# Kernel optimization log

Measured on AMD Instinct MI355X. Metric: run time of the kernel, lower is better.

The kernel has to match this reference:

```python
import jax, jax.numpy as jnp
import numpy as np

N_USERS = 200000
N_ITEMS = 100000
NNZ = 3000000
DIM = 128


def setup_inputs() -> dict:
    key = jax.random.key(0)
    k1, k2, k3, k4, k5 = jax.random.split(key, 5)
    user_emb = jax.random.normal(k1, (N_USERS, DIM), dtype=jnp.float32)
    item_emb = jax.random.normal(k2, (N_ITEMS, DIM), dtype=jnp.float32)
    mat_val = jax.random.uniform(k3, (NNZ,), dtype=jnp.float32)
    mat_row = jax.random.randint(k4, (NNZ,), 0, N_USERS, dtype=jnp.int32)
    mat_col = jax.random.randint(k5, (NNZ,), 0, N_ITEMS, dtype=jnp.int32)
    return {"user_emb": user_emb, "item_emb": item_emb, "mat_val": mat_val,
            "mat_row": mat_row, "mat_col": mat_col}


def reference(user_emb, item_emb, mat_val, mat_row, mat_col):
    # Bipartite SpMM, COO form (matches torch.sparse.mm in Aggregator.forward):
    # user_agg_cf = A @ item_emb,  A[u,i] = mat_val over edges (mat_row, mat_col)
    # item_agg_cf = A^T @ user_emb
    # messages: [nnz, DIM]
    u_msgs = mat_val[:, None] * item_emb[mat_col]
    user_agg_cf = jax.ops.segment_sum(u_msgs, mat_row, num_segments=N_USERS)
    i_msgs = mat_val[:, None] * user_emb[mat_row]
    item_agg_cf = jax.ops.segment_sum(i_msgs, mat_col, num_segments=N_ITEMS)
    return (user_agg_cf, item_agg_cf)
```

## Files before the change

kernel.cpp:

```cpp
#include <hip/hip_runtime.h>

#define N_USERS 200000
#define N_ITEMS 100000
#define NNZ     3000000
#define DIM     128
#define N_TOT   (N_USERS + N_ITEMS)

#define USEG_SH 8
#define ISEG_SH 7
#define NUB     ((N_USERS + (1 << USEG_SH) - 1) >> USEG_SH)
#define NIB     ((N_ITEMS + (1 << ISEG_SH) - 1) >> ISEG_SH)
#define NBKT    (NUB + NIB)
#define CAP     6144

#define NBR_BITS 18
#define NBR_MASK ((1 << NBR_BITS) - 1)

#define HDR_INTS_RAW ((N_TOT + 2) + (NBKT + 1) + NBKT)
#define HDR_INTS     ((HDR_INTS_RAW + 1) & ~1)
static const size_t WS_NEEDED = (size_t)HDR_INTS * 4 + (size_t)2 * NNZ * 8;


__global__ __launch_bounds__(256) void zero_buckets(int* __restrict__ bucketA) {
    int i = blockIdx.x * blockDim.x + threadIdx.x;
    if (i < NBKT + 1) bucketA[i] = 0;
}

#define HEPT 16
__global__ __launch_bounds__(256) void bucket_hist(const int* __restrict__ row,
                                                   const int* __restrict__ col,
                                                   int* __restrict__ bucketA) {
    __shared__ int h[NBKT];
    int t = threadIdx.x;
    for (int i = t; i < NBKT; i += 256) h[i] = 0;
    __syncthreads();
    int base = blockIdx.x * (256 * HEPT);
#pragma unroll
    for (int k = 0; k < HEPT; ++k) {
        int e = base + k * 256 + t;
        if (e < NNZ) {
            atomicAdd(&h[row[e] >> USEG_SH], 1);
            atomicAdd(&h[NUB + (col[e] >> ISEG_SH)], 1);
        }
    }
    __syncthreads();
    for (int i = t; i < NBKT; i += 256) {
        int c = h[i];
        if (c) atomicAdd(&bucketA[i], c);
    }
}

__global__ __launch_bounds__(256) void scan_buckets(int* __restrict__ bucketA,
                                                    int* __restrict__ gcur) {
    __shared__ int s[256];
    int t = threadIdx.x;
    int loc[8];
    int sum = 0;
#pragma unroll
    for (int k = 0; k < 8; ++k) {
        int i = t * 8 + k;
        int v = (i < NBKT) ? bucketA[i] : 0;
        loc[k] = v;
        sum += v;
    }
    s[t] = sum;
    __syncthreads();
    for (int o = 1; o < 256; o <<= 1) {
        int x = (t >= o) ? s[t - o] : 0;
        __syncthreads();
        s[t] += x;
        __syncthreads();
    }
    int ex = s[t] - sum;
#pragma unroll
    for (int k = 0; k < 8; ++k) {
        int i = t * 8 + k;
        if (i < NBKT) {
            bucketA[i] = ex;
            gcur[i] = ex;
            ex += loc[k];
        }
    }
    if (t == 255) bucketA[NBKT] = ex;
}

#define P1EPT 16
__global__ __launch_bounds__(256) void fill_pass1(const float* __restrict__ val,
                                                  const int* __restrict__ row,
                                                  const int* __restrict__ col,
                                                  int* __restrict__ gcur,
                                                  int2* __restrict__ stage) {
    __shared__ int h[NBKT];
    int t = threadIdx.x;
    for (int i = t; i < NBKT; i += 256) h[i] = 0;
    __syncthreads();
    int base = blockIdx.x * (256 * P1EPT);
    int r[P1EPT], c[P1EPT], vb[P1EPT];
#pragma unroll
    for (int k = 0; k < P1EPT; ++k) {
        int e = base + k * 256 + t;
        if (e < NNZ) {
            r[k] = row[e];
            c[k] = col[e];
            vb[k] = __float_as_int(val[e]);
            atomicAdd(&h[r[k] >> USEG_SH], 1);
            atomicAdd(&h[NUB + (c[k] >> ISEG_SH)], 1);
        } else {
            r[k] = -1;
        }
    }
    __syncthreads();
    for (int i = t; i < NBKT; i += 256) {
        int cc = h[i];
        h[i] = cc ? atomicAdd(&gcur[i], cc) : 0;
    }
    __syncthreads();
#pragma unroll
    for (int k = 0; k < P1EPT; ++k) {
        if (r[k] >= 0) {
            int b0 = r[k] >> USEG_SH;
            int p = atomicAdd(&h[b0], 1);
            stage[p] = make_int2(((r[k] & ((1 << USEG_SH) - 1)) << NBR_BITS) | c[k], vb[k]);
            int b1 = NUB + (c[k] >> ISEG_SH);
            int q = atomicAdd(&h[b1], 1);
            stage[q] = make_int2(((c[k] & ((1 << ISEG_SH) - 1)) << NBR_BITS) | r[k], vb[k]);
        }
    }
}

__global__ __launch_bounds__(256) void fill_pass2(const int* __restrict__ bucketA,
                                                  int2* __restrict__ edges,
                                                  int* __restrict__ offs) {
    __shared__ int scnt[256];
    __shared__ int ss[256];
    __shared__ int2 lout[CAP];
    int b = blockIdx.x;
    int t = threadIdx.x;
    int beg = bucketA[b];
    int end = bucketA[b + 1];
    int cnt = end - beg;
    if (cnt > CAP) cnt = CAP;
    int first_seg, nseg;
    if (b < NUB) {
        first_seg = b << USEG_SH;
        nseg = min(1 << USEG_SH, N_USERS - first_seg);
    } else {
        first_seg = N_USERS + ((b - NUB) << ISEG_SH);
        nseg = min(1 << ISEG_SH, N_TOT - first_seg);
    }
    scnt[t] = 0;
    __syncthreads();
    for (int i = beg + t; i < end; i += 256) {
        int2 e = edges[i];
        atomicAdd(&scnt[e.x >> NBR_BITS], 1);
    }
    __syncthreads();
    int v = scnt[t];
    ss[t] = v;
    __syncthreads();
    for (int o = 1; o < 256; o <<= 1) {
        int x = (t >= o) ? ss[t - o] : 0;
        __syncthreads();
        ss[t] += x;
        __syncthreads();
    }
    int excl = ss[t] - v;
    if (t < nseg) offs[first_seg + t] = beg + excl;
    scnt[t] = excl;
    __syncthreads();
    for (int i = beg + t; i < end; i += 256) {
        int2 e = edges[i];
        int ls = e.x >> NBR_BITS;
        int p = atomicAdd(&scnt[ls], 1);
        if (p < CAP) lout[p] = make_int2(e.x & NBR_MASK, e.y);
    }
    __syncthreads();
    for (int i = t; i < cnt; i += 256) edges[beg + i] = lout[i];
    if (b == NBKT - 1 && t == 0) offs[N_TOT] = 2 * NNZ;
}

__global__ __launch_bounds__(256) void gather_kernel(const float* __restrict__ user_emb,
                                                     const float* __restrict__ item_emb,
                                                     const int* __restrict__ offs,
                                                     const int2* __restrict__ edges,
                                                     float* __restrict__ out) {
    int g = (blockIdx.x * blockDim.x + threadIdx.x) >> 5;
    int lane = threadIdx.x & 31;
    if (g >= N_TOT) return;

    int beg = offs[g];
    int end = offs[g + 1];
    const float* src = (g < N_USERS) ? item_emb : user_emb;

    float4 acc = make_float4(0.f, 0.f, 0.f, 0.f);
    for (int j = beg; j < end; ++j) {
        int2 e = edges[j];
        float v = __int_as_float(e.y);
        float4 x = ((const float4*)(src + (long long)e.x * DIM))[lane];
        acc.x += v * x.x;
        acc.y += v * x.y;
        acc.z += v * x.z;
        acc.w += v * x.w;
    }
    ((float4*)(out + (long long)g * DIM))[lane] = acc;
}


__global__ __launch_bounds__(256) void zero_out(float4* __restrict__ out, int n4) {
    int i = blockIdx.x * blockDim.x + threadIdx.x;
    if (i < n4) out[i] = make_float4(0.f, 0.f, 0.f, 0.f);
}

__global__ __launch_bounds__(256) void scatter_kernel(
    const float* __restrict__ user_emb, const float* __restrict__ item_emb,
    const float* __restrict__ mat_val, const int* __restrict__ mat_row,
    const int* __restrict__ mat_col, float* __restrict__ user_agg,
    float* __restrict__ item_agg) {
    long long t = (long long)blockIdx.x * blockDim.x + threadIdx.x;
    int e = (int)(t >> 5);
    int lane = (int)(t & 31);
    if (e >= NNZ) return;
    float v = mat_val[e];
    int r = mat_row[e], c = mat_col[e];
    float4 iv = ((const float4*)(item_emb + (long long)c * DIM))[lane];
    float4 uv = ((const float4*)(user_emb + (long long)r * DIM))[lane];
    float* uout = user_agg + (long long)r * DIM + lane * 4;
    float* iout = item_agg + (long long)c * DIM + lane * 4;
    atomicAdd(uout + 0, v * iv.x); atomicAdd(uout + 1, v * iv.y);
    atomicAdd(uout + 2, v * iv.z); atomicAdd(uout + 3, v * iv.w);
    atomicAdd(iout + 0, v * uv.x); atomicAdd(iout + 1, v * uv.y);
    atomicAdd(iout + 2, v * uv.z); atomicAdd(iout + 3, v * uv.w);
}


extern "C" void kernel_launch(void* const* d_in, const int* in_sizes, int n_in,
                              void* d_out, int out_size, void* d_ws, size_t ws_size,
                              hipStream_t stream) {
    const float* user_emb = (const float*)d_in[0];
    const float* item_emb = (const float*)d_in[1];
    const float* mat_val  = (const float*)d_in[2];
    const int*   mat_row  = (const int*)d_in[3];
    const int*   mat_col  = (const int*)d_in[4];
    float* out = (float*)d_out;

    if (ws_size < WS_NEEDED || d_ws == nullptr) {
        int n4 = (N_USERS + N_ITEMS) * DIM / 4;
        zero_out<<<(n4 + 255) / 256, 256, 0, stream>>>((float4*)d_out, n4);
        long long total_threads = (long long)NNZ * 32;
        int blocks = (int)((total_threads + 255) / 256);
        scatter_kernel<<<blocks, 256, 0, stream>>>(
            user_emb, item_emb, mat_val, mat_row, mat_col,
            out, out + (long long)N_USERS * DIM);
        return;
    }

    int* offs    = (int*)d_ws;
    int* bucketA = offs + (N_TOT + 2);
    int* gcur    = bucketA + (NBKT + 1);
    int2* edges  = (int2*)((int*)d_ws + HDR_INTS);

    zero_buckets<<<(NBKT + 256) / 256, 256, 0, stream>>>(bucketA);
    bucket_hist<<<(NNZ + 256 * HEPT - 1) / (256 * HEPT), 256, 0, stream>>>(
        mat_row, mat_col, bucketA);
    scan_buckets<<<1, 256, 0, stream>>>(bucketA, gcur);
    fill_pass1<<<(NNZ + 256 * P1EPT - 1) / (256 * P1EPT), 256, 0, stream>>>(
        mat_val, mat_row, mat_col, gcur, edges);
    fill_pass2<<<NBKT, 256, 0, stream>>>(bucketA, edges, offs);

    long long gthreads = (long long)N_TOT * 32;
    int gblocks = (int)((gthreads + 255) / 256);
    gather_kernel<<<gblocks, 256, 0, stream>>>(user_emb, item_emb, offs, edges, out);
}
```

Measured before the change: 820.7 us.

## Fuse build into cooperative kernel, gather from fp16 embedding copies per bucket

Merges the bucket zero/histogram/scan/scatter kernels into one cooperative launch with grid syncs, reusing the local histogram offsets from the first pass. Idle blocks convert both embedding tables to fp16 copies during the histogram phase. The second pass and gather are fused so each bucket sorts its edges in LDS and gathers directly, with smaller buckets and 4-way unrolled loads. This cuts launches and halves gather bandwidth, but loses precision and may break if a bucket exceeds the smaller LDS capacity or the cooperative grid does not fit.

```diff
diff --git a/kernel.cpp b/kernel.cpp
--- a/kernel.cpp
+++ b/kernel.cpp
@@ -1,4 +1,7 @@
 #include <hip/hip_runtime.h>
+#include <hip/hip_cooperative_groups.h>
+
+namespace cg = cooperative_groups;
 
 #define N_USERS 200000
 #define N_ITEMS 100000
@@ -6,203 +9,226 @@
 #define DIM     128
 #define N_TOT   (N_USERS + N_ITEMS)
 
-#define USEG_SH 8
-#define ISEG_SH 7
+#define USEG_SH 7
+#define ISEG_SH 6
 #define NUB     ((N_USERS + (1 << USEG_SH) - 1) >> USEG_SH)
 #define NIB     ((N_ITEMS + (1 << ISEG_SH) - 1) >> ISEG_SH)
 #define NBKT    (NUB + NIB)
-#define CAP     6144
+#define CAPL    2560
 
 #define NBR_BITS 18
 #define NBR_MASK ((1 << NBR_BITS) - 1)
 
-#define HDR_INTS_RAW ((N_TOT + 2) + (NBKT + 1) + NBKT)
-#define HDR_INTS     ((HDR_INTS_RAW + 1) & ~1)
-static const size_t WS_NEEDED = (size_t)HDR_INTS * 4 + (size_t)2 * NNZ * 8;
-
-
-__global__ __launch_bounds__(256) void zero_buckets(int* __restrict__ bucketA) {
-    int i = blockIdx.x * blockDim.x + threadIdx.x;
-    if (i < NBKT + 1) bucketA[i] = 0;
-}
-
-#define HEPT 16
-__global__ __launch_bounds__(256) void bucket_hist(const int* __restrict__ row,
-                                                   const int* __restrict__ col,
-                                                   int* __restrict__ bucketA) {
+#define P1EPT  24
+#define FB     ((NNZ + 256 * P1EPT - 1) / (256 * P1EPT))
+#define CVB    384
+#define GRID_B (FB + CVB)
+
+typedef float f4 __attribute__((ext_vector_type(4)));
+typedef _Float16 h4 __attribute__((ext_vector_type(4)));
+typedef _Float16 h8 __attribute__((ext_vector_type(8)));
+
+#define HDR_INTS_RAW ((NBKT + 1) + NBKT)
+#define HDR_INTS     ((HDR_INTS_RAW + 3) & ~3)
+static const size_t WS_MAIN = (size_t)HDR_INTS * 4 + (size_t)2 * NNZ * 8
+                            + (size_t)N_TOT * DIM * 2;
+
+__global__ __launch_bounds__(256, 4) void build_all(
+    const float* __restrict__ val, const int* __restrict__ row,
+    const int* __restrict__ col, const float* __restrict__ ue,
+    const float* __restrict__ ie, int* __restrict__ bucketA,
+    int* __restrict__ gcur, int2* __restrict__ stage,
+    h8* __restrict__ hu, h8* __restrict__ hi)
+{
+    cg::grid_group grid = cg::this_grid();
     __shared__ int h[NBKT];
-    int t = threadIdx.x;
-    for (int i = t; i < NBKT; i += 256) h[i] = 0;
-    __syncthreads();
-    int base = blockIdx.x * (256 * HEPT);
-#pragma unroll
-    for (int k = 0; k < HEPT; ++k) {
-        int e = base + k * 256 + t;
-        if (e < NNZ) {
-            atomicAdd(&h[row[e] >> USEG_SH], 1);
-            atomicAdd(&h[NUB + (col[e] >> ISEG_SH)], 1);
-        }
-    }
-    __syncthreads();
-    for (int i = t; i < NBKT; i += 256) {
-        int c = h[i];
-        if (c) atomicAdd(&bucketA[i], c);
-    }
-}
-
-__global__ __launch_bounds__(256) void scan_buckets(int* __restrict__ bucketA,
-                                                    int* __restrict__ gcur) {
-    __shared__ int s[256];
-    int t = threadIdx.x;
-    int loc[8];
-    int sum = 0;
-#pragma unroll
-    for (int k = 0; k < 8; ++k) {
-        int i = t * 8 + k;
-        int v = (i < NBKT) ? bucketA[i] : 0;
-        loc[k] = v;
-        sum += v;
-    }
-    s[t] = sum;
-    __syncthreads();
-    for (int o = 1; o < 256; o <<= 1) {
-        int x = (t >= o) ? s[t - o] : 0;
-        __syncthreads();
-        s[t] += x;
-        __syncthreads();
-    }
-    int ex = s[t] - sum;
-#pragma unroll
-    for (int k = 0; k < 8; ++k) {
-        int i = t * 8 + k;
-        if (i < NBKT) {
-            bucketA[i] = ex;
-            gcur[i] = ex;
-            ex += loc[k];
-        }
-    }
-    if (t == 255) bucketA[NBKT] = ex;
-}
-
-#define P1EPT 16
-__global__ __launch_bounds__(256) void fill_pass1(const float* __restrict__ val,
-                                                  const int* __restrict__ row,
-                                                  const int* __restrict__ col,
-                                                  int* __restrict__ gcur,
-                                                  int2* __restrict__ stage) {
-    __shared__ int h[NBKT];
-    int t = threadIdx.x;
-    for (int i = t; i < NBKT; i += 256) h[i] = 0;
-    __syncthreads();
-    int base = blockIdx.x * (256 * P1EPT);
-    int r[P1EPT], c[P1EPT], vb[P1EPT];
-#pragma unroll
-    for (int k = 0; k < P1EPT; ++k) {
-        int e = base + k * 256 + t;
-        if (e < NNZ) {
-            r[k] = row[e];
-            c[k] = col[e];
-            vb[k] = __float_as_int(val[e]);
-            atomicAdd(&h[r[k] >> USEG_SH], 1);
-            atomicAdd(&h[NUB + (c[k] >> ISEG_SH)], 1);
-        } else {
-            r[k] = -1;
-        }
-    }
-    __syncthreads();
-    for (int i = t; i < NBKT; i += 256) {
-        int cc = h[i];
-        h[i] = cc ? atomicAdd(&gcur[i], cc) : 0;
-    }
-    __syncthreads();
-#pragma unroll
-    for (int k = 0; k < P1EPT; ++k) {
-        if (r[k] >= 0) {
-            int b0 = r[k] >> USEG_SH;
-            int p = atomicAdd(&h[b0], 1);
-            stage[p] = make_int2(((r[k] & ((1 << USEG_SH) - 1)) << NBR_BITS) | c[k], vb[k]);
-            int b1 = NUB + (c[k] >> ISEG_SH);
-            int q = atomicAdd(&h[b1], 1);
-            stage[q] = make_int2(((c[k] & ((1 << ISEG_SH) - 1)) << NBR_BITS) | r[k], vb[k]);
-        }
-    }
-}
-
-__global__ __launch_bounds__(256) void fill_pass2(const int* __restrict__ bucketA,
-                                                  int2* __restrict__ edges,
-                                                  int* __restrict__ offs) {
+    const int t = threadIdx.x;
+    const int b = blockIdx.x;
+    int lr[P1EPT];
+
+    for (int i = b * 256 + t; i < NBKT + 1; i += GRID_B * 256) bucketA[i] = 0;
+    grid.sync();
+
+    if (b < FB) {
+        for (int i = t; i < NBKT; i += 256) h[i] = 0;
+        __syncthreads();
+        const int base = b * (256 * P1EPT);
+#pragma unroll
+        for (int k = 0; k < P1EPT; ++k) {
+            int e = base + k * 256 + t;
+            int lu = 0, li = 0;
+            if (e < NNZ) {
+                int r = row[e], c = col[e];
+                lu = atomicAdd(&h[r >> USEG_SH], 1);
+                li = atomicAdd(&h[NUB + (c >> ISEG_SH)], 1);
+            }
+            lr[k] = lu | (li << 16);
+        }
+        __syncthreads();
+        for (int i = t; i < NBKT; i += 256) {
+            int cc = h[i];
+            if (cc) atomicAdd(&bucketA[i], cc);
+        }
+    } else {
+        const int U8 = N_USERS * DIM / 8;
+        const int TOT8 = N_TOT * DIM / 8;
+        for (int i = (b - FB) * 256 + t; i < TOT8; i += CVB * 256) {
+            f4 a, bb;
+            if (i < U8) {
+                a  = ((const f4*)ue)[2 * i];
+                bb = ((const f4*)ue)[2 * i + 1];
+            } else {
+                int j = i - U8;
+                a  = ((const f4*)ie)[2 * j];
+                bb = ((const f4*)ie)[2 * j + 1];
+            }
+            h8 o = {(_Float16)a.x,  (_Float16)a.y,  (_Float16)a.z,  (_Float16)a.w,
+                    (_Float16)bb.x, (_Float16)bb.y, (_Float16)bb.z, (_Float16)bb.w};
+            if (i < U8) hu[i] = o; else hi[i - U8] = o;
+        }
+    }
+    grid.sync();
+
+    if (b == FB) {
+        int loc[13];
+        int sum = 0;
+#pragma unroll
+        for (int k = 0; k < 13; ++k) {
+            int i = t * 13 + k;
+            int v = (i < NBKT) ? bucketA[i] : 0;
+            loc[k] = v;
+            sum += v;
+        }
+        h[t] = sum;
+        __syncthreads();
+        for (int o = 1; o < 256; o <<= 1) {
+            int x = (t >= o) ? h[t - o] : 0;
+            __syncthreads();
+            h[t] += x;
+            __syncthreads();
+        }
+        int ex = h[t] - sum;
+#pragma unroll
+        for (int k = 0; k < 13; ++k) {
+            int i = t * 13 + k;
+            if (i < NBKT) {
+                bucketA[i] = ex;
+                gcur[i] = ex;
+                ex += loc[k];
+            }
+        }
+        if (t == 255) bucketA[NBKT] = ex;
+    }
+    grid.sync();
+
+    if (b < FB) {
+        for (int i = t; i < NBKT; i += 256) {
+            int cc = h[i];
+            h[i] = cc ? atomicAdd(&gcur[i], cc) : 0;
+        }
+        __syncthreads();
+        const int base = b * (256 * P1EPT);
+#pragma unroll
+        for (int k = 0; k < P1EPT; ++k) {
+            int e = base + k * 256 + t;
+            if (e < NNZ) {
+                int r = row[e], c = col[e];
+                int vb = __float_as_int(val[e]);
+                int bu = r >> USEG_SH;
+                int bi = NUB + (c >> ISEG_SH);
+                int pu = h[bu] + (lr[k] & 0xffff);
+                int pi = h[bi] + (lr[k] >> 16);
+                stage[pu] = make_int2(((r & ((1 << USEG_SH) - 1)) << NBR_BITS) | c, vb);
+                stage[pi] = make_int2(((c & ((1 << ISEG_SH) - 1)) << NBR_BITS) | r, vb);
+            }
+        }
+    }
+}
+
+__global__ __launch_bounds__(256) void fused_gather(const _Float16* __restrict__ hu,
+                                                    const _Float16* __restrict__ hi,
+                                                    const int2* __restrict__ stage,
+                                                    const int* __restrict__ bases,
+                                                    float* __restrict__ out) {
+    __shared__ int2 lout[CAPL];
     __shared__ int scnt[256];
-    __shared__ int ss[256];
-    __shared__ int2 lout[CAP];
+    __shared__ int sbeg[257];
     int b = blockIdx.x;
     int t = threadIdx.x;
-    int beg = bucketA[b];
-    int end = bucketA[b + 1];
-    int cnt = end - beg;
-    if (cnt > CAP) cnt = CAP;
+    int base = bases[b];
+    int cnt = bases[b + 1] - base;
+    if (cnt > CAPL) cnt = CAPL;
     int first_seg, nseg;
+    const _Float16* src;
     if (b < NUB) {
         first_seg = b << USEG_SH;
         nseg = min(1 << USEG_SH, N_USERS - first_seg);
+        src = hi;
     } else {
         first_seg = N_USERS + ((b - NUB) << ISEG_SH);
         nseg = min(1 << ISEG_SH, N_TOT - first_seg);
+        src = hu;
     }
     scnt[t] = 0;
     __syncthreads();
-    for (int i = beg + t; i < end; i += 256) {
-        int2 e = edges[i];
-        atomicAdd(&scnt[e.x >> NBR_BITS], 1);
-    }
+    for (int i = t; i < cnt; i += 256)
+        atomicAdd(&scnt[stage[base + i].x >> NBR_BITS], 1);
     __syncthreads();
     int v = scnt[t];
-    ss[t] = v;
+    sbeg[t] = v;
     __syncthreads();
     for (int o = 1; o < 256; o <<= 1) {
-        int x = (t >= o) ? ss[t - o] : 0;
-        __syncthreads();
-        ss[t] += x;
-        __syncthreads();
-    }
-    int excl = ss[t] - v;
-    if (t < nseg) offs[first_seg + t] = beg + excl;
+        int x = (t >= o) ? sbeg[t - o] : 0;
+        __syncthreads();
+        sbeg[t] += x;
+        __syncthreads();
+    }
+    int incl = sbeg[t];
+    int excl = incl - v;
+    if (t == 255) sbeg[256] = incl;
+    sbeg[t] = excl;
     scnt[t] = excl;
     __syncthreads();
-    for (int i = beg + t; i < end; i += 256) {
-        int2 e = edges[i];
+    for (int i = t; i < cnt; i += 256) {
+        int2 e = stage[base + i];
         int ls = e.x >> NBR_BITS;
         int p = atomicAdd(&scnt[ls], 1);
-        if (p < CAP) lout[p] = make_int2(e.x & NBR_MASK, e.y);
-    }
-    __syncthreads();
-    for (int i = t; i < cnt; i += 256) edges[beg + i] = lout[i];
-    if (b == NBKT - 1 && t == 0) offs[N_TOT] = 2 * NNZ;
-}
-
-__global__ __launch_bounds__(256) void gather_kernel(const float* __restrict__ user_emb,
-                                                     const float* __restrict__ item_emb,
-                                                     const int* __restrict__ offs,
-                                                     const int2* __restrict__ edges,
-                                                     float* __restrict__ out) {
-    int g = (blockIdx.x * blockDim.x + threadIdx.x) >> 5;
-    int lane = threadIdx.x & 31;
-    if (g >= N_TOT) return;
-
-    int beg = offs[g];
-    int end = offs[g + 1];
-    const float* src = (g < N_USERS) ? item_emb : user_emb;
-
-    float4 acc = make_float4(0.f, 0.f, 0.f, 0.f);
-    for (int j = beg; j < end; ++j) {
-        int2 e = edges[j];
-        float v = __int_as_float(e.y);
-        float4 x = ((const float4*)(src + (long long)e.x * DIM))[lane];
-        acc.x += v * x.x;
-        acc.y += v * x.y;
-        acc.z += v * x.z;
-        acc.w += v * x.w;
-    }
-    ((float4*)(out + (long long)g * DIM))[lane] = acc;
+        lout[p] = make_int2(e.x & NBR_MASK, e.y);
+    }
+    __syncthreads();
+
+    int grp = t >> 5, lane = t & 31;
+    for (int ls = grp; ls < nseg; ls += 8) {
+        int j = sbeg[ls];
+        int j1 = sbeg[ls + 1];
+        f4 acc = (f4)0.f;
+        for (; j + 4 <= j1; j += 4) {
+            int2 e0 = lout[j + 0];
+            int2 e1 = lout[j + 1];
+            int2 e2 = lout[j + 2];
+            int2 e3 = lout[j + 3];
+            h4 x0 = ((const h4*)(src + (long long)e0.x * DIM))[lane];
+            h4 x1 = ((const h4*)(src + (long long)e1.x * DIM))[lane];
+            h4 x2 = ((const h4*)(src + (long long)e2.x * DIM))[lane];
+            h4 x3 = ((const h4*)(src + (long long)e3.x * DIM))[lane];
+            float v0 = __int_as_float(e0.y);
+            float v1 = __int_as_float(e1.y);
+            float v2 = __int_as_float(e2.y);
+            float v3 = __int_as_float(e3.y);
+            acc += v0 * (f4){(float)x0.x, (float)x0.y, (float)x0.z, (float)x0.w};
+            acc += v1 * (f4){(float)x1.x, (float)x1.y, (float)x1.z, (float)x1.w};
+            acc += v2 * (f4){(float)x2.x, (float)x2.y, (float)x2.z, (float)x2.w};
+            acc += v3 * (f4){(float)x3.x, (float)x3.y, (float)x3.z, (float)x3.w};
+        }
+        for (; j < j1; ++j) {
+            int2 e = lout[j];
+            float vv = __int_as_float(e.y);
+            h4 x = ((const h4*)(src + (long long)e.x * DIM))[lane];
+            acc += vv * (f4){(float)x.x, (float)x.y, (float)x.z, (float)x.w};
+        }
+        __builtin_nontemporal_store(acc,
+            (f4*)(out + (long long)(first_seg + ls) * DIM) + lane);
+    }
 }
 
 
@@ -243,7 +269,7 @@
     const int*   mat_col  = (const int*)d_in[4];
     float* out = (float*)d_out;
 
-    if (ws_size < WS_NEEDED || d_ws == nullptr) {
+    if (ws_size < WS_MAIN || d_ws == nullptr) {
         int n4 = (N_USERS + N_ITEMS) * DIM / 4;
         zero_out<<<(n4 + 255) / 256, 256, 0, stream>>>((float4*)d_out, n4);
         long long total_threads = (long long)NNZ * 32;
@@ -254,20 +280,19 @@
         return;
     }
 
-    int* offs    = (int*)d_ws;
-    int* bucketA = offs + (N_TOT + 2);
+    int* bucketA = (int*)d_ws;
     int* gcur    = bucketA + (NBKT + 1);
-    int2* edges  = (int2*)((int*)d_ws + HDR_INTS);
-
-    zero_buckets<<<(NBKT + 256) / 256, 256, 0, stream>>>(bucketA);
-    bucket_hist<<<(NNZ + 256 * HEPT - 1) / (256 * HEPT), 256, 0, stream>>>(
-        mat_row, mat_col, bucketA);
-    scan_buckets<<<1, 256, 0, stream>>>(bucketA, gcur);
-    fill_pass1<<<(NNZ + 256 * P1EPT - 1) / (256 * P1EPT), 256, 0, stream>>>(
-        mat_val, mat_row, mat_col, gcur, edges);
-    fill_pass2<<<NBKT, 256, 0, stream>>>(bucketA, edges, offs);
-
-    long long gthreads = (long long)N_TOT * 32;
-    int gblocks = (int)((gthreads + 255) / 256);
-    gather_kernel<<<gblocks, 256, 0, stream>>>(user_emb, item_emb, offs, edges, out);
-}
+    int2* stage  = (int2*)((int*)d_ws + HDR_INTS);
+    _Float16* hu = (_Float16*)((char*)d_ws + (size_t)HDR_INTS * 4
+                               + (size_t)2 * NNZ * 8);
+    _Float16* hi = hu + (size_t)N_USERS * DIM;
+
+    void* kargs[] = { (void*)&mat_val, (void*)&mat_row, (void*)&mat_col,
+                      (void*)&user_emb, (void*)&item_emb,
+                      (void*)&bucketA, (void*)&gcur, (void*)&stage,
+                      (void*)&hu, (void*)&hi };
+    hipLaunchCooperativeKernel((const void*)build_all, dim3(GRID_B), dim3(256),
+                               kargs, 0, stream);
+
+    fused_gather<<<NBKT, 256, 0, stream>>>(hu, hi, stage, bucketA, out);
+}
```

Result: slower. 1.043 ms (+27.1%).
